# Kernel optimization log

Hardware: AMD Instinct MI355X
Metric: run time of the kernel (lower is better)

## Reference

```python
import jax, jax.numpy as jnp
import numpy as np

B, L, D, K = 32, 512, 512, 3
LOG_2PI = float(np.log(2.0 * np.pi))


def conv1d(x, w, b):
    # x: (B, L, 1), w: (D, 1, K), b: (D,) -> (B, L, D); padding = (K-1)//2
    pad = (w.shape[-1] - 1) // 2
    y = jax.lax.conv_general_dilated(
        x.transpose(0, 2, 1), w, window_strides=(1,), padding=[(pad, pad)],
        dimension_numbers=('NCH', 'OIH', 'NCH'))
    return y.transpose(0, 2, 1) + b


def setup_inputs() -> dict:
    ks = jax.random.split(jax.random.key(0), 14)
    x = jax.random.normal(ks[0], (B, L, D), dtype=jnp.float32)
    durations_float = jax.random.uniform(ks[1], (B, L), dtype=jnp.float32) * 8.0
    durations_int = jax.random.randint(ks[2], (B, L), 1, 8, dtype=jnp.int32)
    energies = jax.random.normal(ks[3], (B, L), dtype=jnp.float32)
    pitch = jax.random.normal(ks[4], (B, L), dtype=jnp.float32)
    input_lengths = jax.random.randint(ks[5], (B,), L // 2, L + 1, dtype=jnp.int32)
    input_lengths = input_lengths.at[0].set(L)  # ensure max length == L (torch masks at max(lengths))
    s = 0.05
    w_dur = jax.random.normal(ks[6], (D, 1, K), dtype=jnp.float32) * s
    b_dur = jax.random.normal(ks[7], (D,), dtype=jnp.float32) * s
    w_en = jax.random.normal(ks[8], (D, 1, K), dtype=jnp.float32) * s
    b_en = jax.random.normal(ks[9], (D,), dtype=jnp.float32) * s
    w_pitch = jax.random.normal(ks[10], (D, 1, K), dtype=jnp.float32) * s
    b_pitch = jax.random.normal(ks[11], (D,), dtype=jnp.float32) * s
    w_lin = jax.random.normal(ks[12], (1, D), dtype=jnp.float32) * s
    b_lin = jax.random.normal(ks[13], (1,), dtype=jnp.float32) * s
    nb_frames = int(jnp.max(jnp.cumsum(durations_int, axis=1)))  # concrete static T
    return dict(x=x, durations_float=durations_float, durations_int=durations_int,
                energies=energies, pitch=pitch, input_lengths=input_lengths,
                w_dur=w_dur, b_dur=b_dur, w_en=w_en, b_en=b_en,
                w_pitch=w_pitch, b_pitch=b_pitch, w_lin=w_lin, b_lin=b_lin,
                nb_frames=nb_frames)


def reference(x, durations_float, durations_int, energies, pitch, input_lengths,
              w_dur, b_dur, w_en, b_en, w_pitch, b_pitch, w_lin, b_lin, nb_frames):
    Bb, Ll, Dd = x.shape
    dur_e = conv1d(durations_float[..., None], w_dur, b_dur)   # (B, L, D)
    en_e = conv1d(energies[..., None], w_en, b_en)
    pi_e = conv1d(pitch[..., None], w_pitch, b_pitch)
    x = x + en_e + pi_e
    range_inputs = x + dur_e
    ranges = jax.nn.softplus(range_inputs @ w_lin.T + b_lin)[..., 0]  # (B, L)
    valid = jnp.arange(Ll) < input_lengths[:, None]                   # (B, L) True = valid
    ranges = jnp.where(valid, ranges, 1.0)
    d = durations_int.astype(x.dtype)
    cumsum = jnp.cumsum(durations_int, axis=1)
    means = d * 0.5 + jnp.concatenate(
        [jnp.zeros((Bb, 1), x.dtype), cumsum[:, :-1].astype(x.dtype)], axis=1)  # (B, L)
    frames = jnp.arange(nb_frames, dtype=x.dtype) + 0.5                # (T,)
    z = (frames[None, None, :] - means[..., None]) / ranges[..., None] # (B, L, T)
    log_probs = -0.5 * z * z - jnp.log(ranges)[..., None] - 0.5 * LOG_2PI
    probs = jnp.where(valid[..., None], jnp.exp(log_probs), 0.0)       # (B, L, T)
    weights = probs / (jnp.sum(probs, axis=1, keepdims=True) + 1e-20)
    # torch: sum_L x[b,l,d] * w[b,l,t] -> (B, D, T), then permute -> (B, T, D)
    x_upsamp = jnp.einsum('bld,blt->btd', x, weights)
    return x_upsamp, weights
```

## Files before the change

kernel.cpp:

```cpp
#include <hip/hip_runtime.h>
#include <hip/hip_bf16.h>
#include <stdint.h>

#define NB 32
#define NL 512
#define ND 512

typedef __bf16 bf16x8 __attribute__((ext_vector_type(8)));
typedef float  f32x4  __attribute__((ext_vector_type(4)));

__device__ __forceinline__ unsigned short f2bf(float f) {
    uint32_t u = __float_as_uint(f);
    u = (u + 0x7fffu + ((u >> 16) & 1u)) >> 16;
    return (unsigned short)u;
}


__global__ __launch_bounds__(256) void fuse2_kernel(
    const float* __restrict__ x, const float* __restrict__ df,
    const float* __restrict__ en, const float* __restrict__ pi,
    const int* __restrict__ lens,
    const float* __restrict__ w_dur, const float* __restrict__ b_dur,
    const float* __restrict__ w_en,  const float* __restrict__ b_en,
    const float* __restrict__ w_pi,  const float* __restrict__ b_pi,
    const float* __restrict__ w_lin, const float* __restrict__ b_lin,
    unsigned short* __restrict__ Xb, float* __restrict__ ranges)
{
    const int blk = blockIdx.x;
    const int b   = blk >> 6;
    const int lb  = (blk & 63) << 3;
    const int tid = threadIdx.x;
    const int d0  = tid << 1;

    float we[2][3], wp[2][3], wd[2][3], bev[2], bpv[2], bdv[2], wl[2];
    #pragma unroll
    for (int q = 0; q < 2; ++q) {
        const int d = d0 + q;
        #pragma unroll
        for (int k = 0; k < 3; ++k) {
            we[q][k] = w_en[d*3+k];
            wp[q][k] = w_pi[d*3+k];
            wd[q][k] = w_dur[d*3+k];
        }
        bev[q] = b_en[d]; bpv[q] = b_pi[d]; bdv[q] = b_dur[d]; wl[q] = w_lin[d];
    }

    float acc[8];
    #pragma unroll
    for (int i = 0; i < 8; ++i) acc[i] = 0.f;

    uint4 chunk[2];
    unsigned short* cu = (unsigned short*)chunk;

    #pragma unroll
    for (int li = 0; li < 8; ++li) {
        const int l  = lb + li;
        const int bl = (b << 9) + l;
        const float dm1 = (l > 0)      ? df[bl-1] : 0.f;
        const float dc  = df[bl];
        const float dp1 = (l < NL-1)   ? df[bl+1] : 0.f;
        const float em1 = (l > 0)      ? en[bl-1] : 0.f;
        const float ec  = en[bl];
        const float ep1 = (l < NL-1)   ? en[bl+1] : 0.f;
        const float pm1 = (l > 0)      ? pi[bl-1] : 0.f;
        const float pc  = pi[bl];
        const float pp1 = (l < NL-1)   ? pi[bl+1] : 0.f;
        const float2 xv = *(const float2*)&x[(size_t)bl * ND + d0];
        #pragma unroll
        for (int q = 0; q < 2; ++q) {
            const float ev  = we[q][0]*em1 + we[q][1]*ec + we[q][2]*ep1 + bev[q];
            const float pv  = wp[q][0]*pm1 + wp[q][1]*pc + wp[q][2]*pp1 + bpv[q];
            const float xxv = (q ? xv.y : xv.x) + ev + pv;
            cu[q*8 + li] = f2bf(xxv);
            const float dv  = wd[q][0]*dm1 + wd[q][1]*dc + wd[q][2]*dp1 + bdv[q];
            acc[li] += (xxv + dv) * wl[q];
        }
    }
    #pragma unroll
    for (int q = 0; q < 2; ++q) {
        const int d = d0 + q;
        const size_t off = (size_t)b * (NL * ND)
            + (size_t)(((lb >> 5) << 5) + (d >> 4)) * 512
            + (size_t)((((lb >> 3) & 3) << 4) + (d & 15)) * 8;
        *(uint4*)&Xb[off] = chunk[q];
    }

    #pragma unroll
    for (int li = 0; li < 8; ++li)
        #pragma unroll
        for (int off = 32; off; off >>= 1)
            acc[li] += __shfl_down(acc[li], off, 64);
    __shared__ float red[4][8];
    const int lane = tid & 63, wid = tid >> 6;
    if (lane == 0)
        #pragma unroll
        for (int li = 0; li < 8; ++li) red[wid][li] = acc[li];
    __syncthreads();
    if (tid < 8) {
        const float s = red[0][tid] + red[1][tid] + red[2][tid] + red[3][tid] + b_lin[0];
        float r = fmaxf(s, 0.f) + log1pf(expf(-fabsf(s)));
        if (lb + tid >= lens[b]) r = 1.0f;
        ranges[(b << 9) + lb + tid] = r;
    }
}


#define C2F 0.84932180028801904272f

#define GENP5(kk, buf) do {                                                     \
    const int l0_ = (kk) * 32 + oct * 4;                                        \
    float pv_[4];                                                               \
    unsigned short pu_[4];                                                      \
    _Pragma("unroll")                                                           \
    for (int j = 0; j < 4; ++j) {                                               \
        const float u_ = fmaf(ftv, t_a[l0_ + j], t_b[l0_ + j]);                 \
        pv_[j] = t_sc[l0_ + j] * exp2f(-u_ * u_);                               \
        pu_[j] = f2bf(pv_[j]);                                                  \
    }                                                                           \
    char* pd_ = smem + (buf) * 4096 + (tloc >> 4) * 1024                        \
              + (((oct >> 1) << 4) + (tloc & 15)) * 16 + ((oct & 1) << 3);      \
    *(uint2*)pd_ = *(uint2*)pu_;                                                \
    if (tvalid) {                                                               \
        _Pragma("unroll")                                                       \
        for (int j = 0; j < 4; ++j)                                             \
            woutb[(size_t)(l0_ + j) * T] = pv_[j] * myDinv;                     \
    }                                                                           \
} while (0)

__global__ __launch_bounds__(512, 4) void fusedwg5_kernel(
    const unsigned short* __restrict__ Xb,
    const float* __restrict__ ranges, const int* __restrict__ di,
    const int* __restrict__ lens,
    float* __restrict__ wout, float* __restrict__ xup, int T)
{
    __shared__ __align__(16) char smem[39424];
    float* t_a   = (float*)(smem + 33024);
    float* t_b   = (float*)(smem + 35072);
    float* t_sc  = (float*)(smem + 37120);
    float* dinvL = (float*)(smem + 39168);
    int*   scanA = (int*)smem;
    int*   scanB = (int*)(smem + 2048);
    float* partial = (float*)(smem + 4096);

    const int tid  = threadIdx.x;
    const int lane = tid & 63, wid = tid >> 6;
    const int wn   = wid;

    const int i    = blockIdx.x;
    const int xcd  = i & 7, slot = i >> 3;
    const int b    = (xcd << 2) + (slot & 3);
    const int m    = slot >> 2;
    const int m64  = m << 6;

    const int tloc = tid & 63;
    const int oct  = tid >> 6;
    const int tglb = m64 + tloc;
    const bool tvalid = tglb < T;
    const float ftv = (float)tglb + 0.5f;

    const char* Bbase = (const char*)Xb + (size_t)b * (NL * ND * 2)
                      + (size_t)(wn << 2) * 1024 + lane * 16;

    bf16x8 bxc[4], bxn[4];
    #pragma unroll
    for (int jj = 0; jj < 4; ++jj)
        bxc[jj] = *(const bf16x8*)(Bbase + jj * 1024);

    const int dv = di[(b << 9) + tid];
    scanA[tid] = dv;
    __syncthreads();
    {
        int* src = scanA; int* dst = scanB;
        #pragma unroll
        for (int off = 1; off < NL; off <<= 1) {
            dst[tid] = src[tid] + (tid >= off ? src[tid - off] : 0);
            __syncthreads();
            int* tmp = src; src = dst; dst = tmp;
        }
        const float mu = (float)src[tid] - 0.5f * (float)dv;
        const float r  = ranges[(b << 9) + tid];
        const float inv = 1.f / r;
        t_a[tid]  = inv * C2F;
        t_b[tid]  = -mu * inv * C2F;
        t_sc[tid] = (tid < lens[b]) ? 0.3989422804014327f * inv : 0.f;
    }
    __syncthreads();

    {
        float s = 0.f;
        const int lbeg = oct << 6;
        #pragma unroll 4
        for (int l = lbeg; l < lbeg + 64; ++l) {
            const float u = fmaf(ftv, t_a[l], t_b[l]);
            s += t_sc[l] * exp2f(-u * u);
        }
        partial[(oct << 6) + tloc] = s;
    }
    __syncthreads();
    if (tid < 64) {
        float sum = 0.f;
        #pragma unroll
        for (int o = 0; o < 8; ++o) sum += partial[(o << 6) + tid];
        dinvL[tid] = 1.f / (sum + 1e-20f);
    }
    __syncthreads();
    const float myDinv = dinvL[tloc];
    float* woutb = wout + (size_t)(b << 9) * T + tglb;

    f32x4 acc[4][4];
    #pragma unroll
    for (int ii = 0; ii < 4; ++ii)
        #pragma unroll
        for (int jj = 0; jj < 4; ++jj) acc[ii][jj] = (f32x4){0.f, 0.f, 0.f, 0.f};

    GENP5(0, 0);

    #pragma unroll
    for (int k = 0; k < 16; ++k) {
        asm volatile("s_waitcnt lgkmcnt(0)" ::: "memory");
        __builtin_amdgcn_s_barrier();
        __builtin_amdgcn_sched_barrier(0);
        const int cur = k & 1;
        if (k < 15) {
            #pragma unroll
            for (int jj = 0; jj < 4; ++jj)
                bxn[jj] = *(const bf16x8*)(Bbase + (size_t)(k + 1) * 32768 + jj * 1024);
            GENP5(k + 1, cur ^ 1);
        }
        bf16x8 af[4];
        #pragma unroll
        for (int ii = 0; ii < 4; ++ii)
            af[ii] = *(const bf16x8*)(smem + cur * 4096 + ii * 1024 + lane * 16);
        #pragma unroll
        for (int ii = 0; ii < 4; ++ii)
            #pragma unroll
            for (int jj = 0; jj < 4; ++jj)
                acc[ii][jj] = __builtin_amdgcn_mfma_f32_16x16x32_bf16(af[ii], bxc[jj], acc[ii][jj], 0, 0, 0);
        #pragma unroll
        for (int jj = 0; jj < 4; ++jj) bxc[jj] = bxn[jj];
    }

    float* lf = (float*)smem;
    float* Ob = xup + (size_t)b * T * ND;
    #pragma unroll
    for (int c = 0; c < 4; ++c) {
        __syncthreads();
        #pragma unroll
        for (int jj = 0; jj < 4; ++jj)
            #pragma unroll
            for (int r = 0; r < 4; ++r) {
                const int row = ((lane >> 4) << 2) + r;
                const int col = (wn << 6) + (jj << 4) + (lane & 15);
                lf[row * 516 + col] = acc[c][jj][r];
            }
        __syncthreads();
        const int trow = tid >> 7;
        const int colq = (tid & 127) << 2;
        #pragma unroll
        for (int s = 0; s < 4; ++s) {
            const int row = trow + (s << 2);
            const int t = m64 + (c << 4) + row;
            if (t < T) {
                const float dsc = dinvL[(c << 4) + row];
                f32x4 v = *(const f32x4*)(lf + row * 516 + colq);
                v[0] *= dsc; v[1] *= dsc; v[2] *= dsc; v[3] *= dsc;
                *(f32x4*)&Ob[(size_t)t * ND + colq] = v;
            }
        }
    }
}

__global__ __launch_bounds__(512) void means_kernel(
    const int* __restrict__ di, float* __restrict__ means)
{
    const int b = blockIdx.x;
    const int l = threadIdx.x;
    __shared__ int s[NL];
    const int d = di[b * NL + l];
    s[l] = d;
    __syncthreads();
    #pragma unroll
    for (int off = 1; off < NL; off <<= 1) {
        const int v = (l >= off) ? s[l - off] : 0;
        __syncthreads();
        s[l] += v;
        __syncthreads();
    }
    means[b * NL + l] = 0.5f * (float)d + (float)(s[l] - d);
}

__global__ __launch_bounds__(256) void fuse_kernel(
    const float* __restrict__ x, const float* __restrict__ df,
    const float* __restrict__ en, const float* __restrict__ pi,
    const int* __restrict__ lens,
    const float* __restrict__ w_dur, const float* __restrict__ b_dur,
    const float* __restrict__ w_en,  const float* __restrict__ b_en,
    const float* __restrict__ w_pi,  const float* __restrict__ b_pi,
    const float* __restrict__ w_lin, const float* __restrict__ b_lin,
    float* __restrict__ xx, float* __restrict__ ranges)
{
    const int bl = blockIdx.x;
    const int b  = bl >> 9;
    const int l  = bl & (NL - 1);
    const int tid = threadIdx.x;
    const float dm1 = (l > 0)      ? df[bl - 1] : 0.f;
    const float d0  = df[bl];
    const float dp1 = (l < NL - 1) ? df[bl + 1] : 0.f;
    const float em1 = (l > 0)      ? en[bl - 1] : 0.f;
    const float e0  = en[bl];
    const float ep1 = (l < NL - 1) ? en[bl + 1] : 0.f;
    const float pm1 = (l > 0)      ? pi[bl - 1] : 0.f;
    const float p0  = pi[bl];
    const float pp1 = (l < NL - 1) ? pi[bl + 1] : 0.f;
    float acc = 0.f;
    #pragma unroll
    for (int d = tid; d < ND; d += 256) {
        const float xv = x[(size_t)bl * ND + d];
        const float ev = w_en[d*3]*em1 + w_en[d*3+1]*e0 + w_en[d*3+2]*ep1 + b_en[d];
        const float pv = w_pi[d*3]*pm1 + w_pi[d*3+1]*p0 + w_pi[d*3+2]*pp1 + b_pi[d];
        const float xxv = xv + ev + pv;
        xx[(size_t)bl * ND + d] = xxv;
        const float dv = w_dur[d*3]*dm1 + w_dur[d*3+1]*d0 + w_dur[d*3+2]*dp1 + b_dur[d];
        acc += (xxv + dv) * w_lin[d];
    }
    #pragma unroll
    for (int off = 32; off; off >>= 1) acc += __shfl_down(acc, off, 64);
    __shared__ float red[4];
    const int lane = tid & 63, wid = tid >> 6;
    if (lane == 0) red[wid] = acc;
    __syncthreads();
    if (tid == 0) {
        const float s = red[0] + red[1] + red[2] + red[3] + b_lin[0];
        float r = fmaxf(s, 0.f) + log1pf(expf(-fabsf(s)));
        if (l >= lens[b]) r = 1.0f;
        ranges[bl] = r;
    }
}

__global__ __launch_bounds__(256) void weights_kernel(
    const float* __restrict__ ranges, const float* __restrict__ means,
    const int* __restrict__ lens, float* __restrict__ weights, int T)
{
    const int b = blockIdx.y;
    const int t = blockIdx.x * 256 + threadIdx.x;
    __shared__ float sm[NL], sinv[NL], sc[NL];
    const int len = lens[b];
    for (int l = threadIdx.x; l < NL; l += 256) {
        const float r = ranges[b * NL + l];
        const float inv = 1.f / r;
        sm[l] = means[b * NL + l];
        sinv[l] = inv;
        sc[l] = (l < len) ? 0.3989422804014327f * inv : 0.f;
    }
    __syncthreads();
    if (t >= T) return;
    const float ft = (float)t + 0.5f;
    float sum = 0.f;
    #pragma unroll 4
    for (int l = 0; l < NL; ++l) {
        const float z = (ft - sm[l]) * sinv[l];
        sum += sc[l] * __expf(-0.5f * z * z);
    }
    const float dinv = 1.f / (sum + 1e-20f);
    #pragma unroll 4
    for (int l = 0; l < NL; ++l) {
        const float z = (ft - sm[l]) * sinv[l];
        weights[((size_t)b * NL + l) * T + t] = sc[l] * __expf(-0.5f * z * z) * dinv;
    }
}

#define BM 64
#define BN 64
#define BK 16
__global__ __launch_bounds__(256) void gemm_f32_kernel(
    const float* __restrict__ xx, const float* __restrict__ weights,
    float* __restrict__ out, int T)
{
    const int b  = blockIdx.z;
    const int t0 = blockIdx.y * BM;
    const int d0 = blockIdx.x * BN;
    const float* __restrict__ W = weights + (size_t)b * NL * T;
    const float* __restrict__ X = xx + (size_t)b * NL * ND;
    float* __restrict__ O = out + (size_t)b * T * ND;
    __shared__ float As[BK][BM];
    __shared__ float Bs[BK][BN];
    const int tid = threadIdx.x;
    const int tx = tid & 15;
    const int ty = tid >> 4;
    const int lr = tid >> 4;
    const int lc = (tid & 15) * 4;
    const bool vec_ok = (t0 + BM <= T) && ((T & 3) == 0);
    float acc[4][4] = {};
    for (int l0 = 0; l0 < NL; l0 += BK) {
        if (vec_ok) {
            *(float4*)&As[lr][lc] = *(const float4*)&W[(size_t)(l0 + lr) * T + t0 + lc];
        } else {
            #pragma unroll
            for (int j = 0; j < 4; ++j) {
                const int tcol = t0 + lc + j;
                As[lr][lc + j] = (tcol < T) ? W[(size_t)(l0 + lr) * T + tcol] : 0.f;
            }
        }
        *(float4*)&Bs[lr][lc] = *(const float4*)&X[(size_t)(l0 + lr) * ND + d0 + lc];
        __syncthreads();
        #pragma unroll
        for (int k = 0; k < BK; ++k) {
            float a[4], bb[4];
            *(float4*)a  = *(const float4*)&As[k][ty * 4];
            *(float4*)bb = *(const float4*)&Bs[k][tx * 4];
            #pragma unroll
            for (int i = 0; i < 4; ++i)
                #pragma unroll
                for (int j = 0; j < 4; ++j)
                    acc[i][j] += a[i] * bb[j];
        }
        __syncthreads();
    }
    #pragma unroll
    for (int i = 0; i < 4; ++i) {
        const int t = t0 + ty * 4 + i;
        if (t < T)
            *(float4*)&O[(size_t)t * ND + d0 + tx * 4] =
                make_float4(acc[i][0], acc[i][1], acc[i][2], acc[i][3]);
    }
}

extern "C" void kernel_launch(void* const* d_in, const int* in_sizes, int n_in,
                              void* d_out, int out_size, void* d_ws, size_t ws_size,
                              hipStream_t stream) {
    const float* x     = (const float*)d_in[0];
    const float* df    = (const float*)d_in[1];
    const int*   di    = (const int*)  d_in[2];
    const float* en    = (const float*)d_in[3];
    const float* pi    = (const float*)d_in[4];
    const int*   lens  = (const int*)  d_in[5];
    const float* w_dur = (const float*)d_in[6];
    const float* b_dur = (const float*)d_in[7];
    const float* w_en  = (const float*)d_in[8];
    const float* b_en  = (const float*)d_in[9];
    const float* w_pi  = (const float*)d_in[10];
    const float* b_pi  = (const float*)d_in[11];
    const float* w_lin = (const float*)d_in[12];
    const float* b_lin = (const float*)d_in[13];

    const int B = NB, L = NL, D = ND;
    const int T = out_size / (B * (L + D));
    const int MT = (T + 63) / 64;

    float* xup  = (float*)d_out;
    float* wout = xup + (size_t)B * T * D;

    const size_t XbBytes = (size_t)B * L * D * 2;
    const size_t need = XbBytes + (size_t)B * L * sizeof(float);

    if (ws_size >= need) {
        unsigned short* Xb = (unsigned short*)d_ws;
        float* ranges = (float*)(Xb + (size_t)B * L * D);

        hipLaunchKernelGGL(fuse2_kernel, dim3(B * 64), dim3(256), 0, stream,
                           x, df, en, pi, lens, w_dur, b_dur, w_en, b_en,
                           w_pi, b_pi, w_lin, b_lin, Xb, ranges);
        hipLaunchKernelGGL(fusedwg5_kernel, dim3(MT * 32), dim3(512), 0, stream,
                           Xb, ranges, di, lens, wout, xup, T);
    } else {
        float* xx     = (float*)d_ws;
        float* ranges = xx + (size_t)B * L * D;
        float* means  = ranges + (size_t)B * L;
        hipLaunchKernelGGL(fuse_kernel, dim3(B * L), dim3(256), 0, stream,
                           x, df, en, pi, lens, w_dur, b_dur, w_en, b_en,
                           w_pi, b_pi, w_lin, b_lin, xx, ranges);
        hipLaunchKernelGGL(means_kernel, dim3(B), dim3(512), 0, stream, di, means);
        hipLaunchKernelGGL(weights_kernel, dim3((T + 255) / 256, B), dim3(256), 0, stream,
                           ranges, means, lens, wout, T);
        hipLaunchKernelGGL(gemm_f32_kernel, dim3(D / BN, (T + BM - 1) / BM, B), dim3(256), 0, stream,
                           xx, wout, xup, T);
    }
}
```

Measured before the change: 98.94 us.

## Make fused weights-GEMM kernel persistent with atomic work-stealing over tiles

The fused weights/GEMM kernel is turned into a persistent kernel with a fixed grid of 512 blocks that pull (batch, T-tile) work items from a global atomic counter. The counter is reset by the preceding fuse2 kernel. This targets the tail effect and launch granularity of the old one-block-per-tile grid. In exchange it drops the XCD-aware block-to-batch mapping, which may hurt L2 reuse of Xb, and it adds an atomic plus barriers per tile.

```diff
diff --git a/kernel.cpp b/kernel.cpp
--- a/kernel.cpp
+++ b/kernel.cpp
@@ -24,8 +24,11 @@
     const float* __restrict__ w_en,  const float* __restrict__ b_en,
     const float* __restrict__ w_pi,  const float* __restrict__ b_pi,
     const float* __restrict__ w_lin, const float* __restrict__ b_lin,
-    unsigned short* __restrict__ Xb, float* __restrict__ ranges)
-{
+    unsigned short* __restrict__ Xb, float* __restrict__ ranges,
+    unsigned int* __restrict__ work_counter)
+{
+    if (blockIdx.x == 0 && threadIdx.x == 0) *work_counter = 0u;
+
     const int blk = blockIdx.x;
     const int b   = blk >> 6;
     const int lb  = (blk & 63) << 3;
@@ -107,7 +110,7 @@
 
 #define C2F 0.84932180028801904272f
 
-#define GENP5(kk, buf) do {                                                     \
+#define GENP7(kk, buf) do {                                                     \
     const int l0_ = (kk) * 32 + oct * 4;                                        \
     float pv_[4];                                                               \
     unsigned short pu_[4];                                                      \
@@ -127,17 +130,19 @@
     }                                                                           \
 } while (0)
 
-__global__ __launch_bounds__(512, 4) void fusedwg5_kernel(
+__global__ __launch_bounds__(512, 4) void fusedwg7_kernel(
     const unsigned short* __restrict__ Xb,
     const float* __restrict__ ranges, const int* __restrict__ di,
     const int* __restrict__ lens,
-    float* __restrict__ wout, float* __restrict__ xup, int T)
-{
-    __shared__ __align__(16) char smem[39424];
+    float* __restrict__ wout, float* __restrict__ xup, int T, int MT,
+    unsigned int* __restrict__ work_counter)
+{
+    __shared__ __align__(16) char smem[39428];
     float* t_a   = (float*)(smem + 33024);
     float* t_b   = (float*)(smem + 35072);
     float* t_sc  = (float*)(smem + 37120);
     float* dinvL = (float*)(smem + 39168);
+    int*   s_w   = (int*)(smem + 39424);
     int*   scanA = (int*)smem;
     int*   scanB = (int*)(smem + 2048);
     float* partial = (float*)(smem + 4096);
@@ -145,126 +150,133 @@
     const int tid  = threadIdx.x;
     const int lane = tid & 63, wid = tid >> 6;
     const int wn   = wid;
-
-    const int i    = blockIdx.x;
-    const int xcd  = i & 7, slot = i >> 3;
-    const int b    = (xcd << 2) + (slot & 3);
-    const int m    = slot >> 2;
-    const int m64  = m << 6;
-
     const int tloc = tid & 63;
     const int oct  = tid >> 6;
-    const int tglb = m64 + tloc;
-    const bool tvalid = tglb < T;
-    const float ftv = (float)tglb + 0.5f;
-
-    const char* Bbase = (const char*)Xb + (size_t)b * (NL * ND * 2)
-                      + (size_t)(wn << 2) * 1024 + lane * 16;
-
-    bf16x8 bxc[4], bxn[4];
-    #pragma unroll
-    for (int jj = 0; jj < 4; ++jj)
-        bxc[jj] = *(const bf16x8*)(Bbase + jj * 1024);
-
-    const int dv = di[(b << 9) + tid];
-    scanA[tid] = dv;
-    __syncthreads();
-    {
-        int* src = scanA; int* dst = scanB;
-        #pragma unroll
-        for (int off = 1; off < NL; off <<= 1) {
-            dst[tid] = src[tid] + (tid >= off ? src[tid - off] : 0);
+    const int nwork = NB * MT;
+
+    for (;;) {
+        __syncthreads();
+        if (tid == 0) *s_w = (int)atomicAdd(work_counter, 1u);
+        __syncthreads();
+        const int w = *s_w;
+        if (w >= nwork) return;
+
+        const int b   = w / MT;
+        const int m   = w - b * MT;
+        const int m64 = m << 6;
+
+        const int tglb = m64 + tloc;
+        const bool tvalid = tglb < T;
+        const float ftv = (float)tglb + 0.5f;
+
+        const char* Bbase = (const char*)Xb + (size_t)b * (NL * ND * 2)
+                          + (size_t)(wn << 2) * 1024 + lane * 16;
+
+        bf16x8 bxc[4], bxn[4];
+        #pragma unroll
+        for (int jj = 0; jj < 4; ++jj)
+            bxc[jj] = *(const bf16x8*)(Bbase + jj * 1024);
+
+        const int dv = di[(b << 9) + tid];
+        scanA[tid] = dv;
+        __syncthreads();
+        {
+            int* src = scanA; int* dst = scanB;
+            #pragma unroll
+            for (int off = 1; off < NL; off <<= 1) {
+                dst[tid] = src[tid] + (tid >= off ? src[tid - off] : 0);
+                __syncthreads();
+                int* tmp = src; src = dst; dst = tmp;
+            }
+            const float mu = (float)src[tid] - 0.5f * (float)dv;
+            const float r  = ranges[(b << 9) + tid];
+            const float inv = 1.f / r;
+            t_a[tid]  = inv * C2F;
+            t_b[tid]  = -mu * inv * C2F;
+            t_sc[tid] = (tid < lens[b]) ? 0.3989422804014327f * inv : 0.f;
+        }
+        __syncthreads();
+
+        {
+            float s = 0.f;
+            const int lbeg = oct << 6;
+            #pragma unroll 4
+            for (int l = lbeg; l < lbeg + 64; ++l) {
+                const float u = fmaf(ftv, t_a[l], t_b[l]);
+                s += t_sc[l] * exp2f(-u * u);
+            }
+            partial[(oct << 6) + tloc] = s;
+        }
+        __syncthreads();
+        if (tid < 64) {
+            float sum = 0.f;
+            #pragma unroll
+            for (int o = 0; o < 8; ++o) sum += partial[(o << 6) + tid];
+            dinvL[tid] = 1.f / (sum + 1e-20f);
+        }
+        __syncthreads();
+        const float myDinv = dinvL[tloc];
+        float* woutb = wout + (size_t)(b << 9) * T + tglb;
+
+        f32x4 acc[4][4];
+        #pragma unroll
+        for (int ii = 0; ii < 4; ++ii)
+            #pragma unroll
+            for (int jj = 0; jj < 4; ++jj) acc[ii][jj] = (f32x4){0.f, 0.f, 0.f, 0.f};
+
+        GENP7(0, 0);
+
+        #pragma unroll
+        for (int k = 0; k < 16; ++k) {
+            asm volatile("s_waitcnt lgkmcnt(0)" ::: "memory");
+            __builtin_amdgcn_s_barrier();
+            __builtin_amdgcn_sched_barrier(0);
+            const int cur = k & 1;
+            if (k < 15) {
+                #pragma unroll
+                for (int jj = 0; jj < 4; ++jj)
+                    bxn[jj] = *(const bf16x8*)(Bbase + (size_t)(k + 1) * 32768 + jj * 1024);
+                GENP7(k + 1, cur ^ 1);
+            }
+            bf16x8 af[4];
+            #pragma unroll
+            for (int ii = 0; ii < 4; ++ii)
+                af[ii] = *(const bf16x8*)(smem + cur * 4096 + ii * 1024 + lane * 16);
+            #pragma unroll
+            for (int ii = 0; ii < 4; ++ii)
+                #pragma unroll
+                for (int jj = 0; jj < 4; ++jj)
+                    acc[ii][jj] = __builtin_amdgcn_mfma_f32_16x16x32_bf16(af[ii], bxc[jj], acc[ii][jj], 0, 0, 0);
+            #pragma unroll
+            for (int jj = 0; jj < 4; ++jj) bxc[jj] = bxn[jj];
+        }
+
+        float* lf = (float*)smem;
+        float* Ob = xup + (size_t)b * T * ND;
+        #pragma unroll
+        for (int c = 0; c < 4; ++c) {
             __syncthreads();
-            int* tmp = src; src = dst; dst = tmp;
-        }
-        const float mu = (float)src[tid] - 0.5f * (float)dv;
-        const float r  = ranges[(b << 9) + tid];
-        const float inv = 1.f / r;
-        t_a[tid]  = inv * C2F;
-        t_b[tid]  = -mu * inv * C2F;
-        t_sc[tid] = (tid < lens[b]) ? 0.3989422804014327f * inv : 0.f;
-    }
-    __syncthreads();
-
-    {
-        float s = 0.f;
-        const int lbeg = oct << 6;
-        #pragma unroll 4
-        for (int l = lbeg; l < lbeg + 64; ++l) {
-            const float u = fmaf(ftv, t_a[l], t_b[l]);
-            s += t_sc[l] * exp2f(-u * u);
-        }
-        partial[(oct << 6) + tloc] = s;
-    }
-    __syncthreads();
-    if (tid < 64) {
-        float sum = 0.f;
-        #pragma unroll
-        for (int o = 0; o < 8; ++o) sum += partial[(o << 6) + tid];
-        dinvL[tid] = 1.f / (sum + 1e-20f);
-    }
-    __syncthreads();
-    const float myDinv = dinvL[tloc];
-    float* woutb = wout + (size_t)(b << 9) * T + tglb;
-
-    f32x4 acc[4][4];
-    #pragma unroll
-    for (int ii = 0; ii < 4; ++ii)
-        #pragma unroll
-        for (int jj = 0; jj < 4; ++jj) acc[ii][jj] = (f32x4){0.f, 0.f, 0.f, 0.f};
-
-    GENP5(0, 0);
-
-    #pragma unroll
-    for (int k = 0; k < 16; ++k) {
-        asm volatile("s_waitcnt lgkmcnt(0)" ::: "memory");
-        __builtin_amdgcn_s_barrier();
-        __builtin_amdgcn_sched_barrier(0);
-        const int cur = k & 1;
-        if (k < 15) {
             #pragma unroll
             for (int jj = 0; jj < 4; ++jj)
-                bxn[jj] = *(const bf16x8*)(Bbase + (size_t)(k + 1) * 32768 + jj * 1024);
-            GENP5(k + 1, cur ^ 1);
-        }
-        bf16x8 af[4];
-        #pragma unroll
-        for (int ii = 0; ii < 4; ++ii)
-            af[ii] = *(const bf16x8*)(smem + cur * 4096 + ii * 1024 + lane * 16);
-        #pragma unroll
-        for (int ii = 0; ii < 4; ++ii)
-            #pragma unroll
-            for (int jj = 0; jj < 4; ++jj)
-                acc[ii][jj] = __builtin_amdgcn_mfma_f32_16x16x32_bf16(af[ii], bxc[jj], acc[ii][jj], 0, 0, 0);
-        #pragma unroll
-        for (int jj = 0; jj < 4; ++jj) bxc[jj] = bxn[jj];
-    }
-
-    float* lf = (float*)smem;
-    float* Ob = xup + (size_t)b * T * ND;
-    #pragma unroll
-    for (int c = 0; c < 4; ++c) {
-        __syncthreads();
-        #pragma unroll
-        for (int jj = 0; jj < 4; ++jj)
-            #pragma unroll
-            for (int r = 0; r < 4; ++r) {
-                const int row = ((lane >> 4) << 2) + r;
-                const int col = (wn << 6) + (jj << 4) + (lane & 15);
-                lf[row * 516 + col] = acc[c][jj][r];
-            }
-        __syncthreads();
-        const int trow = tid >> 7;
-        const int colq = (tid & 127) << 2;
-        #pragma unroll
-        for (int s = 0; s < 4; ++s) {
-            const int row = trow + (s << 2);
-            const int t = m64 + (c << 4) + row;
-            if (t < T) {
-                const float dsc = dinvL[(c << 4) + row];
-                f32x4 v = *(const f32x4*)(lf + row * 516 + colq);
-                v[0] *= dsc; v[1] *= dsc; v[2] *= dsc; v[3] *= dsc;
-                *(f32x4*)&Ob[(size_t)t * ND + colq] = v;
+                #pragma unroll
+                for (int r = 0; r < 4; ++r) {
+                    const int row = ((lane >> 4) << 2) + r;
+                    const int col = (wn << 6) + (jj << 4) + (lane & 15);
+                    lf[row * 516 + col] = acc[c][jj][r];
+                }
+            __syncthreads();
+            const int trow = tid >> 7;
+            const int colq = (tid & 127) << 2;
+            #pragma unroll
+            for (int s = 0; s < 4; ++s) {
+                const int row = trow + (s << 2);
+                const int t = m64 + (c << 4) + row;
+                if (t < T) {
+                    const float dsc = dinvL[(c << 4) + row];
+                    f32x4 v = *(const f32x4*)(lf + row * 516 + colq);
+                    v[0] *= dsc; v[1] *= dsc; v[2] *= dsc; v[3] *= dsc;
+                    *(f32x4*)&Ob[(size_t)t * ND + colq] = v;
+                }
             }
         }
     }
@@ -451,17 +463,18 @@
     float* wout = xup + (size_t)B * T * D;
 
     const size_t XbBytes = (size_t)B * L * D * 2;
-    const size_t need = XbBytes + (size_t)B * L * sizeof(float);
+    const size_t need = XbBytes + (size_t)B * L * sizeof(float) + 64;
 
     if (ws_size >= need) {
         unsigned short* Xb = (unsigned short*)d_ws;
         float* ranges = (float*)(Xb + (size_t)B * L * D);
+        unsigned int* counter = (unsigned int*)(ranges + (size_t)B * L);
 
         hipLaunchKernelGGL(fuse2_kernel, dim3(B * 64), dim3(256), 0, stream,
                            x, df, en, pi, lens, w_dur, b_dur, w_en, b_en,
-                           w_pi, b_pi, w_lin, b_lin, Xb, ranges);
-        hipLaunchKernelGGL(fusedwg5_kernel, dim3(MT * 32), dim3(512), 0, stream,
-                           Xb, ranges, di, lens, wout, xup, T);
+                           w_pi, b_pi, w_lin, b_lin, Xb, ranges, counter);
+        hipLaunchKernelGGL(fusedwg7_kernel, dim3(512), dim3(512), 0, stream,
+                           Xb, ranges, di, lens, wout, xup, T, MT, counter);
     } else {
         float* xx     = (float*)d_ws;
         float* ranges = xx + (size_t)B * L * D;
```

Measured after the change: 244.5 us. 2.47x slower.
